# Performance work log

Hardware: AMD Instinct MI355X
Metric: run time of the kernel (lower is better)

The kernel has to match this reference:

```python
import jax, jax.numpy as jnp
import numpy as np

V_PATCH_NUMS = (1, 2, 4, 6, 8, 10, 13, 16)
HW = 16
QUANT_RESI = 0.5
SHARE_K = 4
BETA = 1.0


def _pool_matrix(n_in, n_out):
    # adaptive average pooling as a [n_out, n_in] matrix (matches F.adaptive_avg_pool2d bins)
    P = np.zeros((n_out, n_in), np.float32)
    for i in range(n_out):
        s = (i * n_in) // n_out
        e = -((-(i + 1) * n_in) // n_out)  # ceil((i+1)*n_in/n_out)
        P[i, s:e] = 1.0 / (e - s)
    return jnp.asarray(P)


def _phi_index(si, SN):
    # PhiPartiallyShared.__getitem__(si/(SN-1)) with K=4 ticks
    K = SHARE_K
    ticks = np.linspace(1.0 / 3 / K, 1 - 1.0 / 3 / K, K) if K == 4 else np.linspace(1.0 / 2 / K, 1 - 1.0 / 2 / K, K)
    return int(np.argmin(np.abs(ticks - si / (SN - 1))))


def _phi(h, w, b):
    # Phi: h*(1-r) + conv3x3(h)*r, zero padding (nn.Conv2d default)
    y = jax.lax.conv_general_dilated(h, w, (1, 1), 'SAME',
                                     dimension_numbers=('NCHW', 'OIHW', 'NCHW'))
    y = y + b[None, :, None, None]
    return h * (1.0 - QUANT_RESI) + y * QUANT_RESI


def setup_inputs() -> dict:
    key = jax.random.key(0)
    k0, k1, k2 = jax.random.split(key, 3)
    B, C, V = 64, 32, 4096
    f = jax.random.normal(k0, (B, C, HW, HW), jnp.float32)
    embed = jax.random.normal(k1, (V, C), jnp.float32)  # EMAEmbedding.weight ~ randn
    phi_w = jax.random.normal(k2, (SHARE_K, C, C, 3, 3), jnp.float32) * (1.0 / np.sqrt(9.0 * C))
    phi_b = jnp.zeros((SHARE_K, C), jnp.float32)
    return {"f_BChw": f, "embed_weight": embed, "phi_w": phi_w, "phi_b": phi_b}


def reference(f_BChw, embed_weight, phi_w, phi_b):
    B, C, H, W = f_BChw.shape
    SN = len(V_PATCH_NUMS)
    f_ng = jax.lax.stop_gradient(f_BChw)
    f_hat = jnp.zeros_like(f_BChw)
    e_sq = jnp.sum(embed_weight * embed_weight, axis=1)  # [V]
    loss = jnp.float32(0.0)
    for si, pn in enumerate(V_PATCH_NUMS):
        rest = f_ng - jax.lax.stop_gradient(f_hat)  # residual to quantize (no grad through distance)
        if pn != H:
            P = _pool_matrix(H, pn)
            rest_d = jnp.einsum('oh,bchw,pw->bcop', P, rest, P)  # adaptive avg pool -> [B,C,pn,pn]
        else:
            rest_d = rest
        rest_NC = rest_d.transpose(0, 2, 3, 1).reshape(-1, C)  # [B*pn*pn, C]
        # squared euclidean cdist to codebook, argmin
        d = (jnp.sum(rest_NC * rest_NC, axis=1, keepdims=True)
             + e_sq[None, :]
             - 2.0 * (rest_NC @ embed_weight.T))  # [N, V]
        idx = jnp.argmin(d, axis=1)  # [B*pn*pn] int
        h = embed_weight[idx].reshape(B, pn, pn, C).transpose(0, 3, 1, 2)  # gather -> [B,C,pn,pn]
        if pn != H:
            h = jax.image.resize(h, (B, C, H, W), method='linear')  # bilinear, align_corners=False
        k = _phi_index(si, SN)
        h = _phi(h, phi_w[k], phi_b[k])
        f_hat = f_hat + h
        loss = loss + 0.25 * jnp.mean((jax.lax.stop_gradient(f_hat) - f_BChw) ** 2) \
                    + BETA * jnp.mean((f_hat - f_ng) ** 2)
    loss = loss / SN
    # straight-through estimator: grads flow to f_BChw as identity
    f_hat_st = jax.lax.stop_gradient(f_hat - f_BChw) + f_BChw
    return f_hat_st, loss
```

## Files before the change

### kernel.cpp

```cpp
#include <hip/hip_runtime.h>
#include <hip/hip_bf16.h>

#define BB 64
#define CC 32
#define HW2 256
#define VV 4096
#define NELEM (BB*CC*HW2)
#define PADW 18
#define PADA 324

#define OFF_F     0
#define OFF_FHAT  (OFF_F     + NELEM)
#define OFF_EMBT  (OFF_FHAT  + NELEM)
#define OFF_ESQ   (OFF_EMBT  + VV*CC)
#define OFF_PW    (OFF_ESQ   + VV)
#define OFF_PB    (OFF_PW    + 4*CC*CC*9)
#define OFF_REST  (OFF_PB    + 4*CC)
#define OFF_BESTA (OFF_REST  + 16384*CC)
#define OFF_BESTB (OFF_BESTA + 2*16384)
#define OFF_LOSS  (OFF_BESTB + 2*16384)
#define OFF_FLAG  (OFF_LOSS  + 1)

__device__ __forceinline__ int embt_idx(int v, int c) {
    return (v >> 6) * 2048 + c * 64 + (v & 63);
}

__global__ void k_probe(const void* __restrict__ fin, int* __restrict__ flag) {
    __shared__ int cnt[256];
    int t = threadIdx.x;
    const __hip_bfloat16* p = (const __hip_bfloat16*)fin;
    int local = 0;
    for (int i = t; i < 8192; i += 256) {
        float v = __bfloat162float(p[i]);
        if (!(fabsf(v) < 1e3f)) local++;
    }
    cnt[t] = local;
    __syncthreads();
    for (int s = 128; s > 0; s >>= 1) {
        if (t < s) cnt[t] += cnt[t + s];
        __syncthreads();
    }
    if (t == 0) *flag = (cnt[0] >= 64) ? 1 : 0;
}

__global__ void k_prep(const void* __restrict__ fin,
                       const void* __restrict__ ein,
                       const void* __restrict__ win,
                       const void* __restrict__ bin_,
                       const int* __restrict__ flag,
                       float* __restrict__ f, float* __restrict__ fhat,
                       float* __restrict__ embT, float* __restrict__ pw,
                       float* __restrict__ pb, float* __restrict__ loss) {
    bool isf32 = (*flag != 0);
    int i = blockIdx.x * 256 + threadIdx.x;
    if (i < NELEM) {
        f[i] = isf32 ? ((const float*)fin)[i]
                     : __bfloat162float(((const __hip_bfloat16*)fin)[i]);
        fhat[i] = 0.f;
    }
    if (i < VV*CC) {
        float ev = isf32 ? ((const float*)ein)[i]
                         : __bfloat162float(((const __hip_bfloat16*)ein)[i]);
        int v = i >> 5, c = i & 31;
        embT[embt_idx(v, c)] = ev;
    }
    if (i < 4*CC*CC*9)
        pw[i] = isf32 ? ((const float*)win)[i]
                      : __bfloat162float(((const __hip_bfloat16*)win)[i]);
    if (i < 4*CC)
        pb[i] = isf32 ? ((const float*)bin_)[i]
                      : __bfloat162float(((const __hip_bfloat16*)bin_)[i]);
    if (i == 0) *loss = 0.f;
}

__global__ void k_esq(const float* __restrict__ embT, float* __restrict__ esq) {
    int v = blockIdx.x * 256 + threadIdx.x;
    if (v >= VV) return;
    const float* p = embT + (v >> 6) * 2048 + (v & 63);
    float s = 0.f;
    #pragma unroll
    for (int c = 0; c < CC; ++c) { float e = p[c * 64]; s = fmaf(e, e, s); }
    esq[v] = s;
}

__global__ void k_pool0(const float* __restrict__ f, const float* __restrict__ fhat,
                        float* __restrict__ rest, unsigned long long* __restrict__ best) {
    int n = threadIdx.x;
    int c = blockIdx.y;
    if (n >= BB) return;
    if (c == 0) best[n] = 0xFFFFFFFFFFFFFFFFull;
    const float* fb = f + (n * CC + c) * HW2;
    const float* hb = fhat + (n * CC + c) * HW2;
    float s = 0.f;
    for (int h = 0; h < 16; ++h)
        for (int w = 0; w < 16; ++w)
            s += fb[h * 16 + w] - hb[h * 16 + w];
    rest[n * CC + c] = s * (1.f / 256.f);
}

__global__ __launch_bounds__(256)
void k_argmin(const float* __restrict__ rest, const float* __restrict__ embT,
              const float* __restrict__ esq, unsigned long long* __restrict__ best,
              int Ntot, int cpw) {
    __shared__ float xT[CC][132];
    __shared__ float eT[CC * 64];
    __shared__ float xxs[2][128];
    int tid = threadIdx.x;
    int tx = tid & 15, ty = tid >> 4;
    int qblk = blockIdx.x * 128;
    int v0 = blockIdx.y * cpw;
    int t0 = v0 >> 6;

    {
        int q = tid >> 1, h = tid & 1;
        int qq = qblk + q; if (qq > Ntot - 1) qq = Ntot - 1;
        const float* xr = rest + qq * CC + h * 16;
        float part = 0.f;
        #pragma unroll
        for (int c = 0; c < 16; ++c) {
            float xv = xr[c];
            xT[h * 16 + c][q] = xv;
            part = fmaf(xv, xv, part);
        }
        xxs[h][q] = part;
    }
    __syncthreads();

    float xx[8];
    #pragma unroll
    for (int i = 0; i < 8; ++i) {
        int q = ty * 8 + i;
        xx[i] = xxs[0][q] + xxs[1][q];
    }

    float bd[8]; int bi[8];
    #pragma unroll
    for (int i = 0; i < 8; ++i) { bd[i] = 3.4e38f; bi[i] = v0; }

    int ntiles = cpw >> 6;
    for (int t = 0; t < ntiles; ++t) {
        int vbase = v0 + t * 64;
        const float* gt = embT + (size_t)(t0 + t) * 2048;
        float4 s0 = *(const float4*)(gt + tid * 4);
        float4 s1 = *(const float4*)(gt + 1024 + tid * 4);
        __syncthreads();
        *(float4*)(eT + tid * 4) = s0;
        *(float4*)(eT + 1024 + tid * 4) = s1;
        __syncthreads();

        float acc[8][4];
        #pragma unroll
        for (int i = 0; i < 8; ++i)
            #pragma unroll
            for (int j = 0; j < 4; ++j) acc[i][j] = 0.f;

        #pragma unroll 8
        for (int k = 0; k < CC; ++k) {
            float4 a0 = *(const float4*)&xT[k][ty * 8];
            float4 a1 = *(const float4*)&xT[k][ty * 8 + 4];
            float4 b4 = *(const float4*)&eT[k * 64 + tx * 4];
            float a[8] = {a0.x, a0.y, a0.z, a0.w, a1.x, a1.y, a1.z, a1.w};
            float b[4] = {b4.x, b4.y, b4.z, b4.w};
            #pragma unroll
            for (int i = 0; i < 8; ++i)
                #pragma unroll
                for (int j = 0; j < 4; ++j)
                    acc[i][j] = fmaf(a[i], b[j], acc[i][j]);
        }

        float4 es4 = *(const float4*)(esq + vbase + tx * 4);
        float es[4] = {es4.x, es4.y, es4.z, es4.w};
        #pragma unroll
        for (int i = 0; i < 8; ++i) {
            float base = xx[i];
            #pragma unroll
            for (int j = 0; j < 4; ++j) {
                float dist = fmaf(-2.f, acc[i][j], base + es[j]);
                if (dist < bd[i]) { bd[i] = dist; bi[i] = vbase + tx * 4 + j; }
            }
        }
    }

    #pragma unroll
    for (int i = 0; i < 8; ++i) {
        unsigned u = __float_as_uint(bd[i]);
        unsigned long long mono = (u & 0x80000000u)
            ? (unsigned long long)(~u)
            : (unsigned long long)(u | 0x80000000u);
        unsigned long long pk = (mono << 32) | (unsigned long long)(unsigned)bi[i];
        #pragma unroll
        for (int m = 1; m <= 8; m <<= 1) {
            unsigned long long o = __shfl_xor(pk, m, 64);
            if (o < pk) pk = o;
        }
        int q = qblk + ty * 8 + i;
        if (tx == 0 && q < Ntot)
            atomicMin(best + q, pk);
    }
}

__global__ __launch_bounds__(256)
void k_fuse(const float* __restrict__ embT,
            const unsigned long long* __restrict__ best,
            const float* __restrict__ pw, const float* __restrict__ pb,
            const float* __restrict__ f, float* __restrict__ fhat,
            float* __restrict__ loss,
            float* __restrict__ rest,
            unsigned long long* __restrict__ best_next,
            int pn, int k, int pn_next) {
    __shared__ float h_pad[CC * PADA];
    __shared__ float extra[CC * 169];
    __shared__ float red[4];
    int b = blockIdx.x, co8 = blockIdx.y, t = threadIdx.x;
    int nn = pn * pn;
    int y = t >> 4, x = t & 15;

    for (int i = t; i < CC * PADA; i += 256) h_pad[i] = 0.f;

    if (pn == 16) {
        __syncthreads();
        int id = (int)(unsigned)(best[b * HW2 + t] & 0xFFFFFFFFull);
        const float* er = embT + (id >> 6) * 2048 + (id & 63);
        int ctr = (y + 1) * PADW + (x + 1);
        #pragma unroll
        for (int c = 0; c < CC; ++c)
            h_pad[c * PADA + ctr] = er[c * 64];
    } else {
        float (*hs)[169] = (float(*)[169])extra;
        for (int cell = t; cell < nn; cell += 256) {
            int id = (int)(unsigned)(best[b * nn + cell] & 0xFFFFFFFFull);
            const float* er = embT + (id >> 6) * 2048 + (id & 63);
            #pragma unroll
            for (int c = 0; c < CC; ++c) hs[c][cell] = er[c * 64];
        }
        __syncthreads();
        float scale = (float)pn / 16.f;
        float sy = (y + 0.5f) * scale - 0.5f;
        sy = fminf(fmaxf(sy, 0.f), (float)(pn - 1));
        int y0 = (int)sy; int y1 = min(y0 + 1, pn - 1); float wy = sy - (float)y0;
        float sx = (x + 0.5f) * scale - 0.5f;
        sx = fminf(fmaxf(sx, 0.f), (float)(pn - 1));
        int x0 = (int)sx; int x1 = min(x0 + 1, pn - 1); float wx = sx - (float)x0;
        float wy0 = 1.f - wy, wx0 = 1.f - wx;
        int ctr = (y + 1) * PADW + (x + 1);
        #pragma unroll
        for (int c = 0; c < CC; ++c) {
            float v00 = hs[c][y0 * pn + x0], v01 = hs[c][y0 * pn + x1];
            float v10 = hs[c][y1 * pn + x0], v11 = hs[c][y1 * pn + x1];
            float a0 = wy0 * v00 + wy * v10;
            float a1 = wy0 * v01 + wy * v11;
            h_pad[c * PADA + ctr] = wx0 * a0 + wx * a1;
        }
    }
    __syncthreads();

    float acc[4];
    #pragma unroll
    for (int o = 0; o < 4; ++o) acc[o] = 0.f;
    const float* hbase = h_pad + y * PADW + x;
    const float* wpk = pw + (k * CC + co8 * 4) * (CC * 9);
    #pragma unroll
    for (int ci_ = 0; ci_ < CC; ++ci_) {
        float hv[9];
        #pragma unroll
        for (int dy = 0; dy < 3; ++dy)
            #pragma unroll
            for (int dx = 0; dx < 3; ++dx)
                hv[dy * 3 + dx] = hbase[ci_ * PADA + dy * PADW + dx];
        const float* wp = wpk + ci_ * 9;
        #pragma unroll
        for (int o = 0; o < 4; ++o) {
            const float* w9 = wp + o * (CC * 9);
            #pragma unroll
            for (int q = 0; q < 9; ++q) acc[o] = fmaf(hv[q], w9[q], acc[o]);
        }
    }

    float* diff = extra;
    float lsum = 0.f;
    int ctr = (y + 1) * PADW + (x + 1);
    #pragma unroll
    for (int o = 0; o < 4; ++o) {
        int co = co8 * 4 + o;
        float hval = h_pad[co * PADA + ctr];
        float outv = hval * 0.5f + (acc[o] + pb[k * CC + co]) * 0.5f;
        int pos = (b * CC + co) * HW2 + t;
        float fh = fhat[pos] + outv;
        fhat[pos] = fh;
        float dd = f[pos] - fh;
        diff[o * HW2 + t] = dd;
        lsum = fmaf(dd, dd, lsum);
    }
    #pragma unroll
    for (int off = 32; off > 0; off >>= 1) lsum += __shfl_down(lsum, off, 64);
    if ((t & 63) == 0) red[t >> 6] = lsum;
    __syncthreads();
    if (t == 0)
        atomicAdd(loss, red[0] + red[1] + red[2] + red[3]);

    if (pn_next > 0) {
        int nn2 = pn_next * pn_next;
        for (int q = t; q < nn2 * 4; q += 256) {
            int cell = q % nn2, o = q / nn2;
            int i = cell / pn_next, j = cell % pn_next;
            int s0 = (i * 16) / pn_next, e0 = ((i + 1) * 16 + pn_next - 1) / pn_next;
            int s1 = (j * 16) / pn_next, e1 = ((j + 1) * 16 + pn_next - 1) / pn_next;
            float inv = 1.f / (float)((e0 - s0) * (e1 - s1));
            float s = 0.f;
            for (int h = s0; h < e0; ++h)
                for (int w = s1; w < e1; ++w)
                    s += diff[o * HW2 + h * 16 + w];
            rest[(b * nn2 + cell) * CC + co8 * 4 + o] = s * inv;
        }
        if (co8 == 0)
            for (int q = t; q < nn2; q += 256)
                best_next[b * nn2 + q] = 0xFFFFFFFFFFFFFFFFull;
    }
}

__global__ void k_out(const float* __restrict__ fhat, const float* __restrict__ loss,
                      const int* __restrict__ flag, void* __restrict__ out) {
    bool isf32 = (*flag != 0);
    int i = blockIdx.x * 256 + threadIdx.x;
    if (i > NELEM) return;
    float v;
    if (i < NELEM) v = fhat[i];
    else           v = (*loss) * (1.25f / (float)NELEM / 8.f);
    if (isf32) ((float*)out)[i] = v;
    else       ((__hip_bfloat16*)out)[i] = __float2bfloat16(v);
}

extern "C" void kernel_launch(void* const* d_in, const int* in_sizes, int n_in,
                              void* d_out, int out_size, void* d_ws, size_t ws_size,
                              hipStream_t stream) {
    const void* fin  = d_in[0];
    const void* ein  = d_in[1];
    const void* win  = d_in[2];
    const void* bin_ = d_in[3];
    float* ws = (float*)d_ws;
    float* f    = ws + OFF_F;
    float* fhat = ws + OFF_FHAT;
    float* embT = ws + OFF_EMBT;
    float* esq  = ws + OFF_ESQ;
    float* pw   = ws + OFF_PW;
    float* pb   = ws + OFF_PB;
    float* rest = ws + OFF_REST;
    unsigned long long* bestA = (unsigned long long*)(ws + OFF_BESTA);
    unsigned long long* bestB = (unsigned long long*)(ws + OFF_BESTB);
    float* loss = ws + OFF_LOSS;
    int*   flag = (int*)(ws + OFF_FLAG);

    static const int PN[8] = {1, 2, 4, 6, 8, 10, 13, 16};
    static const int KK[8] = {0, 0, 1, 1, 2, 2, 3, 3};
    static const int SP[8] = {64, 64, 64, 64, 32, 32, 16, 16};

    k_probe<<<1, 256, 0, stream>>>(fin, flag);
    k_prep<<<(NELEM + 255) / 256, 256, 0, stream>>>(fin, ein, win, bin_, flag,
                                                    f, fhat, embT, pw, pb, loss);
    k_esq<<<(VV + 255) / 256, 256, 0, stream>>>(embT, esq);
    k_pool0<<<dim3(1, CC), 256, 0, stream>>>(f, fhat, rest, bestA);

    for (int si = 0; si < 8; ++si) {
        int pn = PN[si];
        int Ntot = BB * pn * pn;
        int Sp = SP[si];
        int cpw = VV / Sp;
        unsigned long long* bcur = (si & 1) ? bestB : bestA;
        unsigned long long* bnxt = (si & 1) ? bestA : bestB;
        int pn_next = (si < 7) ? PN[si + 1] : 0;
        int gx = (Ntot + 127) / 128;
        k_argmin<<<dim3(gx, Sp), 256, 0, stream>>>(rest, embT, esq, bcur, Ntot, cpw);
        k_fuse<<<dim3(BB, 8), 256, 0, stream>>>(embT, bcur, pw, pb, f, fhat, loss,
                                                rest, bnxt, pn, KK[si], pn_next);
    }
    k_out<<<(NELEM + 1 + 255) / 256, 256, 0, stream>>>(fhat, loss, flag, d_out);
}
```

Baseline: 462.5 us.

## Restructure argmin kernel to register-resident queries with wave-uniform codebook loads

The argmin kernel no longer stages queries and codebook tiles in shared memory. Each thread now holds two full 32-channel query rows in registers and streams 8 codebook entries per step through wave-uniform (scalar) loads, which removes the LDS traffic and block-wide syncs. The codebook split count per stage is raised a lot to keep the grid full, so more atomicMin traffic lands on the best array. Per-thread reuse of each loaded codebook value falls to two FMAs, so the kernel relies on the scalar-load path being cheap enough.

```diff
diff --git a/kernel.cpp b/kernel.cpp
--- a/kernel.cpp
+++ b/kernel.cpp
@@ -98,105 +98,96 @@
     rest[n * CC + c] = s * (1.f / 256.f);
 }
 
-__global__ __launch_bounds__(256)
+__global__ __launch_bounds__(256, 4)
 void k_argmin(const float* __restrict__ rest, const float* __restrict__ embT,
               const float* __restrict__ esq, unsigned long long* __restrict__ best,
               int Ntot, int cpw) {
-    __shared__ float xT[CC][132];
-    __shared__ float eT[CC * 64];
-    __shared__ float xxs[2][128];
-    int tid = threadIdx.x;
-    int tx = tid & 15, ty = tid >> 4;
-    int qblk = blockIdx.x * 128;
-    int v0 = blockIdx.y * cpw;
-    int t0 = v0 >> 6;
-
+    int tid  = threadIdx.x;
+    int w    = tid >> 6, lane = tid & 63;
+    int q0   = blockIdx.x * 512 + w * 128 + lane;
+    int q1   = q0 + 64;
+    int v0   = blockIdx.y * cpw;
+
+    bool act0 = (q0 < Ntot), act1 = (q1 < Ntot);
+    if (!act0 && !act1) return;
+    int qa = act0 ? q0 : (Ntot - 1);
+    int qb = act1 ? q1 : (Ntot - 1);
+
+    float a0v[32], a1v[32];
     {
-        int q = tid >> 1, h = tid & 1;
-        int qq = qblk + q; if (qq > Ntot - 1) qq = Ntot - 1;
-        const float* xr = rest + qq * CC + h * 16;
-        float part = 0.f;
-        #pragma unroll
-        for (int c = 0; c < 16; ++c) {
-            float xv = xr[c];
-            xT[h * 16 + c][q] = xv;
-            part = fmaf(xv, xv, part);
-        }
-        xxs[h][q] = part;
-    }
-    __syncthreads();
-
-    float xx[8];
-    #pragma unroll
-    for (int i = 0; i < 8; ++i) {
-        int q = ty * 8 + i;
-        xx[i] = xxs[0][q] + xxs[1][q];
-    }
-
-    float bd[8]; int bi[8];
-    #pragma unroll
-    for (int i = 0; i < 8; ++i) { bd[i] = 3.4e38f; bi[i] = v0; }
-
-    int ntiles = cpw >> 6;
+        const float4* ra = (const float4*)(rest + qa * CC);
+        const float4* rb = (const float4*)(rest + qb * CC);
+        #pragma unroll
+        for (int c4 = 0; c4 < 8; ++c4) {
+            float4 va = ra[c4], vb4 = rb[c4];
+            a0v[c4*4+0] = va.x;  a0v[c4*4+1] = va.y;
+            a0v[c4*4+2] = va.z;  a0v[c4*4+3] = va.w;
+            a1v[c4*4+0] = vb4.x; a1v[c4*4+1] = vb4.y;
+            a1v[c4*4+2] = vb4.z; a1v[c4*4+3] = vb4.w;
+        }
+    }
+
+    float p0a = 0.f, p1a = 0.f, p0b = 0.f, p1b = 0.f;
+    #pragma unroll
+    for (int c = 0; c < 16; ++c)  p0a = fmaf(a0v[c], a0v[c], p0a);
+    #pragma unroll
+    for (int c = 16; c < 32; ++c) p1a = fmaf(a0v[c], a0v[c], p1a);
+    #pragma unroll
+    for (int c = 0; c < 16; ++c)  p0b = fmaf(a1v[c], a1v[c], p0b);
+    #pragma unroll
+    for (int c = 16; c < 32; ++c) p1b = fmaf(a1v[c], a1v[c], p1b);
+    float xx0 = p0a + p1a;
+    float xx1 = p0b + p1b;
+
+    float bd0 = 3.4e38f, bd1 = 3.4e38f;
+    int   bi0 = v0,      bi1 = v0;
+
+    int ntiles = cpw >> 3;
     for (int t = 0; t < ntiles; ++t) {
-        int vbase = v0 + t * 64;
-        const float* gt = embT + (size_t)(t0 + t) * 2048;
-        float4 s0 = *(const float4*)(gt + tid * 4);
-        float4 s1 = *(const float4*)(gt + 1024 + tid * 4);
-        __syncthreads();
-        *(float4*)(eT + tid * 4) = s0;
-        *(float4*)(eT + 1024 + tid * 4) = s1;
-        __syncthreads();
-
-        float acc[8][4];
-        #pragma unroll
-        for (int i = 0; i < 8; ++i)
+        int vb = v0 + t * 8;
+        int boff = __builtin_amdgcn_readfirstlane((vb >> 6) * 2048 + (vb & 63));
+        int eoff = __builtin_amdgcn_readfirstlane(vb);
+        const float* bt = embT + boff;
+        const float* ep = esq + eoff;
+
+        float acc0[8], acc1[8];
+        #pragma unroll
+        for (int j = 0; j < 8; ++j) { acc0[j] = 0.f; acc1[j] = 0.f; }
+
+        #pragma unroll
+        for (int k = 0; k < CC; ++k) {
+            float a0 = a0v[k], a1 = a1v[k];
             #pragma unroll
-            for (int j = 0; j < 4; ++j) acc[i][j] = 0.f;
-
-        #pragma unroll 8
-        for (int k = 0; k < CC; ++k) {
-            float4 a0 = *(const float4*)&xT[k][ty * 8];
-            float4 a1 = *(const float4*)&xT[k][ty * 8 + 4];
-            float4 b4 = *(const float4*)&eT[k * 64 + tx * 4];
-            float a[8] = {a0.x, a0.y, a0.z, a0.w, a1.x, a1.y, a1.z, a1.w};
-            float b[4] = {b4.x, b4.y, b4.z, b4.w};
-            #pragma unroll
-            for (int i = 0; i < 8; ++i)
-                #pragma unroll
-                for (int j = 0; j < 4; ++j)
-                    acc[i][j] = fmaf(a[i], b[j], acc[i][j]);
-        }
-
-        float4 es4 = *(const float4*)(esq + vbase + tx * 4);
-        float es[4] = {es4.x, es4.y, es4.z, es4.w};
-        #pragma unroll
-        for (int i = 0; i < 8; ++i) {
-            float base = xx[i];
-            #pragma unroll
-            for (int j = 0; j < 4; ++j) {
-                float dist = fmaf(-2.f, acc[i][j], base + es[j]);
-                if (dist < bd[i]) { bd[i] = dist; bi[i] = vbase + tx * 4 + j; }
+            for (int j = 0; j < 8; ++j) {
+                float bv = bt[k * 64 + j];
+                acc0[j] = fmaf(a0, bv, acc0[j]);
+                acc1[j] = fmaf(a1, bv, acc1[j]);
             }
         }
-    }
-
-    #pragma unroll
-    for (int i = 0; i < 8; ++i) {
-        unsigned u = __float_as_uint(bd[i]);
-        unsigned long long mono = (u & 0x80000000u)
-            ? (unsigned long long)(~u)
-            : (unsigned long long)(u | 0x80000000u);
-        unsigned long long pk = (mono << 32) | (unsigned long long)(unsigned)bi[i];
-        #pragma unroll
-        for (int m = 1; m <= 8; m <<= 1) {
-            unsigned long long o = __shfl_xor(pk, m, 64);
-            if (o < pk) pk = o;
-        }
-        int q = qblk + ty * 8 + i;
-        if (tx == 0 && q < Ntot)
-            atomicMin(best + q, pk);
-    }
+
+        #pragma unroll
+        for (int j = 0; j < 8; ++j) {
+            float es = ep[j];
+            float d0 = fmaf(-2.f, acc0[j], xx0 + es);
+            if (d0 < bd0) { bd0 = d0; bi0 = vb + j; }
+            float d1 = fmaf(-2.f, acc1[j], xx1 + es);
+            if (d1 < bd1) { bd1 = d1; bi1 = vb + j; }
+        }
+    }
+
+    unsigned u0 = __float_as_uint(bd0);
+    unsigned long long mono0 = (u0 & 0x80000000u)
+        ? (unsigned long long)(~u0)
+        : (unsigned long long)(u0 | 0x80000000u);
+    unsigned long long pk0 = (mono0 << 32) | (unsigned long long)(unsigned)bi0;
+    unsigned u1 = __float_as_uint(bd1);
+    unsigned long long mono1 = (u1 & 0x80000000u)
+        ? (unsigned long long)(~u1)
+        : (unsigned long long)(u1 | 0x80000000u);
+    unsigned long long pk1 = (mono1 << 32) | (unsigned long long)(unsigned)bi1;
+
+    if (act0) atomicMin(best + q0, pk0);
+    if (act1) atomicMin(best + q1, pk1);
 }
 
 __global__ __launch_bounds__(256)
@@ -352,7 +343,7 @@
 
     static const int PN[8] = {1, 2, 4, 6, 8, 10, 13, 16};
     static const int KK[8] = {0, 0, 1, 1, 2, 2, 3, 3};
-    static const int SP[8] = {64, 64, 64, 64, 32, 32, 16, 16};
+    static const int SP[8] = {512, 512, 512, 256, 128, 128, 64, 32};
 
     k_probe<<<1, 256, 0, stream>>>(fin, flag);
     k_prep<<<(NELEM + 255) / 256, 256, 0, stream>>>(fin, ein, win, bin_, flag,
@@ -368,7 +359,7 @@
         unsigned long long* bcur = (si & 1) ? bestB : bestA;
         unsigned long long* bnxt = (si & 1) ? bestA : bestB;
         int pn_next = (si < 7) ? PN[si + 1] : 0;
-        int gx = (Ntot + 127) / 128;
+        int gx = (Ntot + 511) / 512;
         k_argmin<<<dim3(gx, Sp), 256, 0, stream>>>(rest, embT, esq, bcur, Ntot, cpw);
         k_fuse<<<dim3(BB, 8), 256, 0, stream>>>(embT, bcur, pw, pb, f, fhat, loss,
                                                 rest, bnxt, pn, KK[si], pn_next);
```

Measured after the change: 447.1 us. -3.3%, faster.
